# Kernel tuning notes

Measured on AMD Instinct MI355X. Metric: run time of the kernel, lower is better.

## Reference

```python
import jax, jax.numpy as jnp
import numpy as np

B, C = 8192, 4096

def _to_complex(r):
    # (..., 2) real/imag stack -> complex
    return jax.lax.complex(r[..., 0], r[..., 1])

def _to_real(z):
    return jnp.stack([jnp.real(z), jnp.imag(z)], axis=-1)

def setup_inputs() -> dict:
    key = jax.random.key(0)
    kx, ka, kd = jax.random.split(key, 3)
    x = jax.random.normal(kx, (B, C, 2), dtype=jnp.float32)
    # A, D ~ Normal(1.0, 0.01) per reset_parameters
    A = 1.0 + 0.01 * jax.random.normal(ka, (1, C, 2), dtype=jnp.float32)
    D = 1.0 + 0.01 * jax.random.normal(kd, (1, C, 2), dtype=jnp.float32)
    return {"x": x, "A": A, "D": D}

def reference(x, A, D):
    # Elementwise scale (real and imag parts scaled independently, NOT complex mul)
    xs = A * x                                   # (B, C, 2)
    # torch.fft(x, 1): complex FFT over the signal dim (channels, dim 1)
    f = jnp.fft.fft(_to_complex(xs), axis=1)     # (B, C) complex64
    fs = D * _to_real(f)                         # elementwise scale in real/imag repr
    # torch.ifft is normalized by 1/N, same as jnp.fft.ifft
    out = jnp.fft.ifft(_to_complex(fs), axis=1)  # (B, C) complex64
    return _to_real(out)                         # (B, C, 2)
```

## Files before the change

### kernel.cpp

```cpp
#include <hip/hip_runtime.h>

#define FFT_N   4096
#define THREADS 256

__device__ __forceinline__ float2 cmul(float2 a, float2 b) {
    return make_float2(a.x*b.x - a.y*b.y, a.x*b.y + a.y*b.x);
}
__device__ __forceinline__ float2 cadd(float2 a, float2 b){ return make_float2(a.x+b.x, a.y+b.y); }
__device__ __forceinline__ float2 csub(float2 a, float2 b){ return make_float2(a.x-b.x, a.y-b.y); }

template<int S>
__device__ __forceinline__ float2 muli(float2 z) {
    return (S < 0) ? make_float2(z.y, -z.x) : make_float2(-z.y, z.x);
}

template<int S>
__device__ __forceinline__ void dft4(float2 a0, float2 a1, float2 a2, float2 a3,
                                     float2& y0, float2& y1, float2& y2, float2& y3) {
    float2 e0 = cadd(a0, a2), e1 = cadd(a1, a3);
    float2 o0 = csub(a0, a2), o1 = muli<S>(csub(a1, a3));
    y0 = cadd(e0, e1); y2 = csub(e0, e1);
    y1 = cadd(o0, o1); y3 = csub(o0, o1);
}

template<int S>
__device__ __forceinline__ void dft16(float2* a) {
    const float C1 = 0.92387953251128674f;
    const float S1 = 0.38268343236508978f;
    const float R2 = 0.70710678118654752f;
    const float sg = (S < 0) ? -1.0f : 1.0f;
    const float2 w1 = make_float2( C1,  sg*S1);
    const float2 w2 = make_float2( R2,  sg*R2);
    const float2 w3 = make_float2( S1,  sg*C1);
    const float2 w6 = make_float2(-R2,  sg*R2);
    const float2 w9 = make_float2(-C1, -sg*S1);
    float2 t[16];
    dft4<S>(a[0], a[4], a[8],  a[12], t[0],  t[1],  t[2],  t[3]);
    dft4<S>(a[1], a[5], a[9],  a[13], t[4],  t[5],  t[6],  t[7]);
    dft4<S>(a[2], a[6], a[10], a[14], t[8],  t[9],  t[10], t[11]);
    dft4<S>(a[3], a[7], a[11], a[15], t[12], t[13], t[14], t[15]);
    t[5]  = cmul(t[5],  w1);  t[6]  = cmul(t[6],  w2);  t[7]  = cmul(t[7],  w3);
    t[9]  = cmul(t[9],  w2);  t[10] = muli<S>(t[10]);   t[11] = cmul(t[11], w6);
    t[13] = cmul(t[13], w3);  t[14] = cmul(t[14], w6);  t[15] = cmul(t[15], w9);
    dft4<S>(t[0], t[4], t[8],  t[12], a[0], a[4], a[8],  a[12]);
    dft4<S>(t[1], t[5], t[9],  t[13], a[1], a[5], a[9],  a[13]);
    dft4<S>(t[2], t[6], t[10], t[14], a[2], a[6], a[10], a[14]);
    dft4<S>(t[3], t[7], t[11], t[15], a[3], a[7], a[11], a[15]);
}

template<int S>
__device__ __forceinline__ void twiddle_apply2(float2* R0, float2* R1, int p, float invM) {
    float ang = 6.283185307179586f * (float)p * invM;
    if (S < 0) ang = -ang;
    float s, c;
    __sincosf(ang, &s, &c);
    float2 w[16];
    w[1] = make_float2(c, s);
    w[2] = cmul(w[1], w[1]);
    w[3] = cmul(w[2], w[1]);
    w[4] = cmul(w[2], w[2]);
    #pragma unroll
    for (int k = 5; k < 16; ++k) w[k] = cmul(w[k-4], w[4]);
    #pragma unroll
    for (int k = 1; k < 16; ++k) {
        R0[k] = cmul(R0[k], w[k]);
        R1[k] = cmul(R1[k], w[k]);
    }
}

__device__ __forceinline__ int swz16(int i) { return i ^ ((i >> 4) & 7); }

__device__ __forceinline__ void wave_lds_fence() {
    asm volatile("s_waitcnt lgkmcnt(0)" ::: "memory");
}

__global__ __launch_bounds__(THREADS, 2) void afdf_fft_kernel(
    const float* __restrict__ x,
    const float* __restrict__ A,
    const float* __restrict__ D,
    float* __restrict__ out)
{
    __shared__ __align__(16) float4 sh[FFT_N];

    const int t = threadIdx.x;
    const size_t rb = (size_t)blockIdx.x * 2 * FFT_N;
    const float2* __restrict__ xr0 = (const float2*)x + rb;
    const float2* __restrict__ xr1 = xr0 + FFT_N;
    const float2* __restrict__ Ac  = (const float2*)A;
    const float2* __restrict__ Dc  = (const float2*)D;
    float2* __restrict__ o0        = (float2*)out + rb;
    float2* __restrict__ o1        = o0 + FFT_N;

    float2 r0[16], r1[16];

    {
        const int p = t;
        #pragma unroll
        for (int n = 0; n < 16; ++n) {
            float2 a  = Ac[p + 256*n];
            float2 v0 = xr0[p + 256*n];
            float2 v1 = xr1[p + 256*n];
            r0[n] = make_float2(a.x*v0.x, a.y*v0.y);
            r1[n] = make_float2(a.x*v1.x, a.y*v1.y);
        }
        dft16<-1>(r0);
        dft16<-1>(r1);
        twiddle_apply2<-1>(r0, r1, p, 1.0f/4096.0f);
        #pragma unroll
        for (int k = 0; k < 16; ++k)
            sh[swz16(p + 256*k)] = make_float4(r0[k].x, r0[k].y, r1[k].x, r1[k].y);
    }
    __syncthreads();

    float2 dreg[16];
    {
        const int k1 = t >> 4, k2 = t & 15;
        const float inv = 1.0f / 4096.0f;
        #pragma unroll
        for (int k3 = 0; k3 < 16; ++k3) {
            float2 d = Dc[256*k3 + 16*k2 + k1];
            dreg[k3] = make_float2(d.x*inv, d.y*inv);
        }
    }
    {
        const int b = t >> 4, p2 = t & 15, base = b*256;
        #pragma unroll
        for (int n = 0; n < 16; ++n) {
            float4 v = sh[swz16(base + p2 + 16*n)];
            r0[n] = make_float2(v.x, v.y);
            r1[n] = make_float2(v.z, v.w);
        }
        dft16<-1>(r0);
        dft16<-1>(r1);
        twiddle_apply2<-1>(r0, r1, p2, 1.0f/256.0f);
        #pragma unroll
        for (int k = 0; k < 16; ++k)
            sh[swz16(base + p2 + 16*k)] = make_float4(r0[k].x, r0[k].y, r1[k].x, r1[k].y);
    }
    wave_lds_fence();

    {
        const int base = 16*t;
        #pragma unroll
        for (int n = 0; n < 16; ++n) {
            float4 v = sh[swz16(base + n)];
            r0[n] = make_float2(v.x, v.y);
            r1[n] = make_float2(v.z, v.w);
        }
        dft16<-1>(r0);
        dft16<-1>(r1);
        #pragma unroll
        for (int k3 = 0; k3 < 16; ++k3) {
            r0[k3] = make_float2(dreg[k3].x*r0[k3].x, dreg[k3].y*r0[k3].y);
            r1[k3] = make_float2(dreg[k3].x*r1[k3].x, dreg[k3].y*r1[k3].y);
        }
        dft16<+1>(r0);
        dft16<+1>(r1);
        #pragma unroll
        for (int n = 0; n < 16; ++n)
            sh[swz16(base + n)] = make_float4(r0[n].x, r0[n].y, r1[n].x, r1[n].y);
    }
    wave_lds_fence();

    {
        const int b = t >> 4, p2 = t & 15, base = b*256;
        #pragma unroll
        for (int k = 0; k < 16; ++k) {
            float4 v = sh[swz16(base + p2 + 16*k)];
            r0[k] = make_float2(v.x, v.y);
            r1[k] = make_float2(v.z, v.w);
        }
        twiddle_apply2<+1>(r0, r1, p2, 1.0f/256.0f);
        dft16<+1>(r0);
        dft16<+1>(r1);
        #pragma unroll
        for (int n = 0; n < 16; ++n)
            sh[swz16(base + p2 + 16*n)] = make_float4(r0[n].x, r0[n].y, r1[n].x, r1[n].y);
    }
    __syncthreads();

    {
        const int p = t;
        #pragma unroll
        for (int k = 0; k < 16; ++k) {
            float4 v = sh[swz16(p + 256*k)];
            r0[k] = make_float2(v.x, v.y);
            r1[k] = make_float2(v.z, v.w);
        }
        twiddle_apply2<+1>(r0, r1, p, 1.0f/4096.0f);
        dft16<+1>(r0);
        dft16<+1>(r1);
        #pragma unroll
        for (int n1 = 0; n1 < 16; ++n1) {
            o0[p + 256*n1] = r0[n1];
            o1[p + 256*n1] = r1[n1];
        }
    }
}

extern "C" void kernel_launch(void* const* d_in, const int* in_sizes, int n_in,
                              void* d_out, int out_size, void* d_ws, size_t ws_size,
                              hipStream_t stream) {
    (void)in_sizes; (void)n_in; (void)out_size; (void)d_ws; (void)ws_size;
    const float* x = (const float*)d_in[0];
    const float* A = (const float*)d_in[1];
    const float* D = (const float*)d_in[2];
    float* out = (float*)d_out;

    afdf_fft_kernel<<<dim3(4096), dim3(THREADS), 0, stream>>>(x, A, D, out);
}
```

Before: 470.4 us.

## Make FFT kernel persistent with register prefetch of next row pair

Launches a fixed grid of 512 blocks that loop over row pairs instead of one block per pair. A and D factors are loaded once per block and kept in registers, and the next pair's input is prefetched into registers during the middle FFT stages to hide global load latency. This adds substantial register pressure, which may cause spills or lower occupancy, and adds an extra block-wide barrier per iteration.

```diff
diff --git a/kernel.cpp b/kernel.cpp
--- a/kernel.cpp
+++ b/kernel.cpp
@@ -2,6 +2,8 @@
 
 #define FFT_N   4096
 #define THREADS 256
+#define GRID_BLOCKS 512
+#define NPAIRS 4096
 
 __device__ __forceinline__ float2 cmul(float2 a, float2 b) {
     return make_float2(a.x*b.x - a.y*b.y, a.x*b.y + a.y*b.x);
@@ -83,37 +85,14 @@
     __shared__ __align__(16) float4 sh[FFT_N];
 
     const int t = threadIdx.x;
-    const size_t rb = (size_t)blockIdx.x * 2 * FFT_N;
-    const float2* __restrict__ xr0 = (const float2*)x + rb;
-    const float2* __restrict__ xr1 = xr0 + FFT_N;
-    const float2* __restrict__ Ac  = (const float2*)A;
-    const float2* __restrict__ Dc  = (const float2*)D;
-    float2* __restrict__ o0        = (float2*)out + rb;
-    float2* __restrict__ o1        = o0 + FFT_N;
-
-    float2 r0[16], r1[16];
-
-    {
-        const int p = t;
-        #pragma unroll
-        for (int n = 0; n < 16; ++n) {
-            float2 a  = Ac[p + 256*n];
-            float2 v0 = xr0[p + 256*n];
-            float2 v1 = xr1[p + 256*n];
-            r0[n] = make_float2(a.x*v0.x, a.y*v0.y);
-            r1[n] = make_float2(a.x*v1.x, a.y*v1.y);
-        }
-        dft16<-1>(r0);
-        dft16<-1>(r1);
-        twiddle_apply2<-1>(r0, r1, p, 1.0f/4096.0f);
-        #pragma unroll
-        for (int k = 0; k < 16; ++k)
-            sh[swz16(p + 256*k)] = make_float4(r0[k].x, r0[k].y, r1[k].x, r1[k].y);
-    }
-    __syncthreads();
-
+    const float2* __restrict__ Ac = (const float2*)A;
+    const float2* __restrict__ Dc = (const float2*)D;
+
+    float2 aA[16];
     float2 dreg[16];
     {
+        #pragma unroll
+        for (int n = 0; n < 16; ++n) aA[n] = Ac[t + 256*n];
         const int k1 = t >> 4, k2 = t & 15;
         const float inv = 1.0f / 4096.0f;
         #pragma unroll
@@ -122,78 +101,126 @@
             dreg[k3] = make_float2(d.x*inv, d.y*inv);
         }
     }
+
+    float2 px0[16], px1[16];
     {
-        const int b = t >> 4, p2 = t & 15, base = b*256;
+        const float2* __restrict__ xr0 = (const float2*)x + (size_t)blockIdx.x * 2 * FFT_N;
+        const float2* __restrict__ xr1 = xr0 + FFT_N;
         #pragma unroll
         for (int n = 0; n < 16; ++n) {
-            float4 v = sh[swz16(base + p2 + 16*n)];
-            r0[n] = make_float2(v.x, v.y);
-            r1[n] = make_float2(v.z, v.w);
-        }
-        dft16<-1>(r0);
-        dft16<-1>(r1);
-        twiddle_apply2<-1>(r0, r1, p2, 1.0f/256.0f);
-        #pragma unroll
-        for (int k = 0; k < 16; ++k)
-            sh[swz16(base + p2 + 16*k)] = make_float4(r0[k].x, r0[k].y, r1[k].x, r1[k].y);
-    }
-    wave_lds_fence();
-
-    {
-        const int base = 16*t;
-        #pragma unroll
-        for (int n = 0; n < 16; ++n) {
-            float4 v = sh[swz16(base + n)];
-            r0[n] = make_float2(v.x, v.y);
-            r1[n] = make_float2(v.z, v.w);
-        }
-        dft16<-1>(r0);
-        dft16<-1>(r1);
-        #pragma unroll
-        for (int k3 = 0; k3 < 16; ++k3) {
-            r0[k3] = make_float2(dreg[k3].x*r0[k3].x, dreg[k3].y*r0[k3].y);
-            r1[k3] = make_float2(dreg[k3].x*r1[k3].x, dreg[k3].y*r1[k3].y);
-        }
-        dft16<+1>(r0);
-        dft16<+1>(r1);
-        #pragma unroll
-        for (int n = 0; n < 16; ++n)
-            sh[swz16(base + n)] = make_float4(r0[n].x, r0[n].y, r1[n].x, r1[n].y);
-    }
-    wave_lds_fence();
-
-    {
-        const int b = t >> 4, p2 = t & 15, base = b*256;
-        #pragma unroll
-        for (int k = 0; k < 16; ++k) {
-            float4 v = sh[swz16(base + p2 + 16*k)];
-            r0[k] = make_float2(v.x, v.y);
-            r1[k] = make_float2(v.z, v.w);
-        }
-        twiddle_apply2<+1>(r0, r1, p2, 1.0f/256.0f);
-        dft16<+1>(r0);
-        dft16<+1>(r1);
-        #pragma unroll
-        for (int n = 0; n < 16; ++n)
-            sh[swz16(base + p2 + 16*n)] = make_float4(r0[n].x, r0[n].y, r1[n].x, r1[n].y);
-    }
-    __syncthreads();
-
-    {
-        const int p = t;
-        #pragma unroll
-        for (int k = 0; k < 16; ++k) {
-            float4 v = sh[swz16(p + 256*k)];
-            r0[k] = make_float2(v.x, v.y);
-            r1[k] = make_float2(v.z, v.w);
-        }
-        twiddle_apply2<+1>(r0, r1, p, 1.0f/4096.0f);
-        dft16<+1>(r0);
-        dft16<+1>(r1);
-        #pragma unroll
-        for (int n1 = 0; n1 < 16; ++n1) {
-            o0[p + 256*n1] = r0[n1];
-            o1[p + 256*n1] = r1[n1];
+            px0[n] = xr0[t + 256*n];
+            px1[n] = xr1[t + 256*n];
+        }
+    }
+
+    float2 r0[16], r1[16];
+
+    #pragma unroll 1
+    for (int pair = blockIdx.x; pair < NPAIRS; pair += GRID_BLOCKS) {
+        float2* __restrict__ o0 = (float2*)out + (size_t)pair * 2 * FFT_N;
+        float2* __restrict__ o1 = o0 + FFT_N;
+
+        {
+            #pragma unroll
+            for (int n = 0; n < 16; ++n) {
+                r0[n] = make_float2(aA[n].x*px0[n].x, aA[n].y*px0[n].y);
+                r1[n] = make_float2(aA[n].x*px1[n].x, aA[n].y*px1[n].y);
+            }
+            dft16<-1>(r0);
+            dft16<-1>(r1);
+            twiddle_apply2<-1>(r0, r1, t, 1.0f/4096.0f);
+            __syncthreads();
+            #pragma unroll
+            for (int k = 0; k < 16; ++k)
+                sh[swz16(t + 256*k)] = make_float4(r0[k].x, r0[k].y, r1[k].x, r1[k].y);
+        }
+        __syncthreads();
+
+        {
+            const int b = t >> 4, p2 = t & 15, base = b*256;
+            #pragma unroll
+            for (int n = 0; n < 16; ++n) {
+                float4 v = sh[swz16(base + p2 + 16*n)];
+                r0[n] = make_float2(v.x, v.y);
+                r1[n] = make_float2(v.z, v.w);
+            }
+            dft16<-1>(r0);
+            dft16<-1>(r1);
+            twiddle_apply2<-1>(r0, r1, p2, 1.0f/256.0f);
+            #pragma unroll
+            for (int k = 0; k < 16; ++k)
+                sh[swz16(base + p2 + 16*k)] = make_float4(r0[k].x, r0[k].y, r1[k].x, r1[k].y);
+        }
+        wave_lds_fence();
+
+        {
+            const int base = 16*t;
+            #pragma unroll
+            for (int n = 0; n < 16; ++n) {
+                float4 v = sh[swz16(base + n)];
+                r0[n] = make_float2(v.x, v.y);
+                r1[n] = make_float2(v.z, v.w);
+            }
+            dft16<-1>(r0);
+            dft16<-1>(r1);
+            #pragma unroll
+            for (int k3 = 0; k3 < 16; ++k3) {
+                r0[k3] = make_float2(dreg[k3].x*r0[k3].x, dreg[k3].y*r0[k3].y);
+                r1[k3] = make_float2(dreg[k3].x*r1[k3].x, dreg[k3].y*r1[k3].y);
+            }
+            dft16<+1>(r0);
+            dft16<+1>(r1);
+            #pragma unroll
+            for (int n = 0; n < 16; ++n)
+                sh[swz16(base + n)] = make_float4(r0[n].x, r0[n].y, r1[n].x, r1[n].y);
+        }
+        wave_lds_fence();
+
+        {
+            const int np = pair + GRID_BLOCKS;
+            if (np < NPAIRS) {
+                const float2* __restrict__ nx0 = (const float2*)x + (size_t)np * 2 * FFT_N;
+                const float2* __restrict__ nx1 = nx0 + FFT_N;
+                #pragma unroll
+                for (int n = 0; n < 16; ++n) {
+                    px0[n] = nx0[t + 256*n];
+                    px1[n] = nx1[t + 256*n];
+                }
+            }
+        }
+
+        {
+            const int b = t >> 4, p2 = t & 15, base = b*256;
+            #pragma unroll
+            for (int k = 0; k < 16; ++k) {
+                float4 v = sh[swz16(base + p2 + 16*k)];
+                r0[k] = make_float2(v.x, v.y);
+                r1[k] = make_float2(v.z, v.w);
+            }
+            twiddle_apply2<+1>(r0, r1, p2, 1.0f/256.0f);
+            dft16<+1>(r0);
+            dft16<+1>(r1);
+            #pragma unroll
+            for (int n = 0; n < 16; ++n)
+                sh[swz16(base + p2 + 16*n)] = make_float4(r0[n].x, r0[n].y, r1[n].x, r1[n].y);
+        }
+        __syncthreads();
+
+        {
+            #pragma unroll
+            for (int k = 0; k < 16; ++k) {
+                float4 v = sh[swz16(t + 256*k)];
+                r0[k] = make_float2(v.x, v.y);
+                r1[k] = make_float2(v.z, v.w);
+            }
+            twiddle_apply2<+1>(r0, r1, t, 1.0f/4096.0f);
+            dft16<+1>(r0);
+            dft16<+1>(r1);
+            #pragma unroll
+            for (int n1 = 0; n1 < 16; ++n1) {
+                o0[t + 256*n1] = r0[n1];
+                o1[t + 256*n1] = r1[n1];
+            }
         }
     }
 }
@@ -207,5 +234,5 @@
     const float* D = (const float*)d_in[2];
     float* out = (float*)d_out;
 
-    afdf_fft_kernel<<<dim3(4096), dim3(THREADS), 0, stream>>>(x, A, D, out);
-}
+    afdf_fft_kernel<<<dim3(GRID_BLOCKS), dim3(THREADS), 0, stream>>>(x, A, D, out);
+}
```

New measurement: 920.6 us. +95.7%, slower.
